# Kernel tuning notes

Measured on AMD Instinct MI355X. Metric: run time of the kernel, lower is better.

## Reference

```python
import jax, jax.numpy as jnp
import numpy as np

H = 64  # lstm hidden size
SLOPE = 0.01  # LeakyReLU default negative slope


def _leaky(x):
    return jnp.where(x >= 0, x, SLOPE * x)


def setup_inputs() -> dict:
    key = jax.random.key(0)
    ks = jax.random.split(key, 20)
    B, T = 32768, 200
    s = 0.1
    inp = {
        "noise": jax.random.normal(ks[0], (B, 3), jnp.float32),
        "w_ih0": jax.random.normal(ks[1], (4 * H, 3), jnp.float32) * s,
        "w_hh0": jax.random.normal(ks[2], (4 * H, H), jnp.float32) * s,
        "b_ih0": jax.random.normal(ks[3], (4 * H,), jnp.float32) * s,
        "b_hh0": jax.random.normal(ks[4], (4 * H,), jnp.float32) * s,
        "w_ih1": jax.random.normal(ks[5], (4 * H, H), jnp.float32) * s,
        "w_hh1": jax.random.normal(ks[6], (4 * H, H), jnp.float32) * s,
        "b_ih1": jax.random.normal(ks[7], (4 * H,), jnp.float32) * s,
        "b_hh1": jax.random.normal(ks[8], (4 * H,), jnp.float32) * s,
        "w_ih2": jax.random.normal(ks[9], (4 * H, H), jnp.float32) * s,
        "w_hh2": jax.random.normal(ks[10], (4 * H, H), jnp.float32) * s,
        "b_ih2": jax.random.normal(ks[11], (4 * H,), jnp.float32) * s,
        "b_hh2": jax.random.normal(ks[12], (4 * H,), jnp.float32) * s,
        "w1": jax.random.normal(ks[13], (32, H), jnp.float32) * s,
        "b1": jax.random.normal(ks[14], (32,), jnp.float32) * s,
        "w2": jax.random.normal(ks[15], (16, 32), jnp.float32) * s,
        "b2": jax.random.normal(ks[16], (16,), jnp.float32) * s,
        "w3": jax.random.normal(ks[17], (3, 16), jnp.float32) * s,
        "b3": jax.random.normal(ks[18], (3,), jnp.float32) * s,
        "length": T,
    }
    return inp


def _forward(noise, w_ih0, w_hh0, b_ih0, b_hh0, w_ih1, w_hh1, b_ih1, b_hh1,
             w_ih2, w_hh2, b_ih2, b_hh2, w1, b1, w2, b2, w3, b3, length):
    B = noise.shape[0]
    layers = [(w_ih0, w_hh0, b_ih0, b_hh0),
              (w_ih1, w_hh1, b_ih1, b_hh1),
              (w_ih2, w_hh2, b_ih2, b_hh2)]

    def cell(x, h, c, wih, whh, bih, bhh):
        # PyTorch LSTM gate order: i, f, g, o
        g = x @ wih.T + h @ whh.T + (bih + bhh)
        i, f, gg, o = jnp.split(g, 4, axis=-1)
        c_new = jax.nn.sigmoid(f) * c + jax.nn.sigmoid(i) * jnp.tanh(gg)
        h_new = jax.nn.sigmoid(o) * jnp.tanh(c_new)
        return h_new, c_new

    def step(carry, _):
        x, hs, cs = carry  # x: (B,3), hs/cs: (3,B,H)
        inp = x
        new_h, new_c = [], []
        for l, (wih, whh, bih, bhh) in enumerate(layers):
            h, c = cell(inp, hs[l], cs[l], wih, whh, bih, bhh)
            new_h.append(h)
            new_c.append(c)
            inp = h
        # MLP head (Dropout is identity in eval; LeakyReLU slope 0.01)
        y = _leaky(inp @ w1.T + b1)
        y = _leaky(y @ w2.T + b2)
        y = _leaky(y @ w3.T + b3)  # (B, 3)
        return (y, jnp.stack(new_h), jnp.stack(new_c)), y

    hs0 = jnp.zeros((3, B, H), noise.dtype)
    cs0 = jnp.zeros((3, B, H), noise.dtype)
    (_, _, _), ys = jax.lax.scan(step, (noise, hs0, cs0), None, length=length)
    return jnp.transpose(ys, (1, 0, 2))  # (B, T, 3)


def reference(noise, w_ih0, w_hh0, b_ih0, b_hh0, w_ih1, w_hh1, b_ih1, b_hh1,
              w_ih2, w_hh2, b_ih2, b_hh2, w1, b1, w2, b2, w3, b3, length):
    return _forward(noise, w_ih0, w_hh0, b_ih0, b_hh0, w_ih1, w_hh1, b_ih1,
                    b_hh1, w_ih2, w_hh2, b_ih2, b_hh2, w1, b1, w2, b2, w3,
                    b3, length)
```

## Files before the change

kernel.cpp:

```cpp
#include <hip/hip_runtime.h>

typedef __attribute__((ext_vector_type(4))) float  f32x4;
typedef __attribute__((ext_vector_type(8))) short  bf16x8;

#define NTHR 1024
#define BT   128
#define L2E  1.4426950408889634f

#define PLANE(L)   ((L)*16384)
#define QBUFP(p)   (49152 + ((p)<<14))
#define XFB_OFF    81920
#define Y1_OFF     83968
#define Y2_OFF     92672
#define W2L_OFF    97280
#define BGL_OFF    98304
#define B1L_OFF    101376
#define B2L_OFF    101504
#define B3L_OFF    101568
#define W3L_OFF    101584
#define W0L_OFF    101776
#define OUT_OFF    105872
#define LDS_TOTAL  112016

__device__ __align__(16) unsigned char g_wsbuf[167936];

__device__ __forceinline__ unsigned short f2bf(float v) {
    unsigned int x = __float_as_uint(v);
    unsigned int r = x + 0x7fffu + ((x >> 16) & 1u);
    return (unsigned short)(r >> 16);
}
__device__ __forceinline__ float bf2f_lo(unsigned int d) { return __uint_as_float(d << 16); }
__device__ __forceinline__ float bf2f_hi(unsigned int d) { return __uint_as_float(d & 0xffff0000u); }

__device__ __forceinline__ float fsig2(float y) {
    return __builtin_amdgcn_rcpf(1.0f + __builtin_amdgcn_exp2f(-y));
}
__device__ __forceinline__ float ftanh2(float y) {
    return 1.0f - 2.0f * __builtin_amdgcn_rcpf(1.0f + __builtin_amdgcn_exp2f(y));
}
__device__ __forceinline__ float ftanhc(float c) {
    return 1.0f - 2.0f * __builtin_amdgcn_rcpf(1.0f + __builtin_amdgcn_exp2f(c * (2.0f * L2E)));
}

__global__ void prep_weights(const float* __restrict__ whh0, const float* __restrict__ wih1,
                             const float* __restrict__ whh1, const float* __restrict__ wih2,
                             const float* __restrict__ whh2, const float* __restrict__ w1g)
{
    int gi = blockIdx.x * 256 + threadIdx.x;
    if (gi < 10240) {
        int m = gi / 2048;
        int rem = gi & 2047;
        int b = rem >> 6, l = rem & 63;
        int ks = b & 1, g = (b >> 1) & 3, ug = b >> 3;
        int row = g * 64 + ug * 16 + (l & 15);
        int kb  = ks * 32 + (l >> 4) * 8;
        float fac = (g == 2) ? (2.0f * L2E) : L2E;
        const float* src = (m == 0) ? whh0 : (m == 1) ? wih1 : (m == 2) ? whh1
                         : (m == 3) ? wih2 : whh2;
        unsigned short o[8];
        #pragma unroll
        for (int i = 0; i < 8; ++i)
            o[i] = f2bf(src[row * 64 + kb + i] * fac);
        unsigned char* dst = g_wsbuf + m * 32768 + b * 1024 + l * 16;
        #pragma unroll
        for (int i = 0; i < 8; ++i) ((unsigned short*)dst)[i] = o[i];
    } else if (gi < 10496) {
        int g2 = gi - 10240;
        int b = g2 >> 6, l = g2 & 63;
        int ks = b & 1, hf = b >> 1;
        int row = hf * 16 + (l & 15);
        int kb  = ks * 32 + (l >> 4) * 8;
        unsigned short o[8];
        #pragma unroll
        for (int i = 0; i < 8; ++i)
            o[i] = f2bf(w1g[row * 64 + kb + i]);
        unsigned char* dst = g_wsbuf + 163840 + b * 1024 + l * 16;
        #pragma unroll
        for (int i = 0; i < 8; ++i) ((unsigned short*)dst)[i] = o[i];
    }
}

#define MFMA_(A,B,C) __builtin_amdgcn_mfma_f32_16x16x32_bf16(A, B, C, 0, 0, 0)

#define BARX do { \
    asm volatile("s_waitcnt lgkmcnt(0)" ::: "memory"); \
    __builtin_amdgcn_s_barrier(); \
    __builtin_amdgcn_sched_barrier(0); \
    } while (0)

#define LOADQ(m, ks, R) \
    R = *(const bf16x8*)(g_wsbuf + (m) * 32768 + \
        ((tid >> 6) * 2 + (ks)) * 1024 + (tid & 63) * 16)
#define COMMITQ(R, p) \
    *(bf16x8*)(lds + QBUFP(p) + tid * 16) = R
#define LOADW1(R) do { if (tid < 256) \
    R = *(const bf16x8*)(g_wsbuf + 163840 + (tid >> 6) * 1024 + (tid & 63) * 16); } while (0)
#define COMMITW1(R, p) do { if (tid < 256) \
    *(bf16x8*)(lds + QBUFP(p) + tid * 16) = R; } while (0)

#define ACC_INIT(L) do { \
    _Pragma("unroll") for (int g_ = 0; g_ < 4; ++g_) { \
        float b_ = *(const float*)(lds + BGL_OFF + ((L) * 256 + g_ * 64 + u) * 4); \
        f32x4 t_ = {b_, b_, b_, b_}; \
        _Pragma("unroll") for (int mt_ = 0; mt_ < 2; ++mt_) acc[g_][mt_] = t_; \
    } } while (0)

#define GATEP(APL, ks, P) do { \
    bf16x8 b_[4]; \
    _Pragma("unroll") for (int g_ = 0; g_ < 4; ++g_) \
        b_[g_] = *(const bf16x8*)(lds + QBUFP(P) + (ug * 4 + g_) * 1024 + lane * 16); \
    _Pragma("unroll") for (int mt_ = 0; mt_ < 2; ++mt_) { \
        int ab_ = (((mbase + mt_ * 16 + l15) * 128 + (ks) * 64 + l4 * 16)) ^ rswz; \
        bf16x8 ah_ = *(const bf16x8*)(lds + PLANE(APL) + ab_); \
        _Pragma("unroll") for (int g_ = 0; g_ < 4; ++g_) \
            acc[g_][mt_] = MFMA_(ah_, b_[g_], acc[g_][mt_]); \
    } } while (0)

#define CELLW(L, CARR) do { \
    _Pragma("unroll") for (int mt_ = 0; mt_ < 2; ++mt_) \
    _Pragma("unroll") for (int r_ = 0; r_ < 4; ++r_) { \
        float gi_ = fsig2(acc[0][mt_][r_]); \
        float gf_ = fsig2(acc[1][mt_][r_]); \
        float gg_ = ftanh2(acc[2][mt_][r_]); \
        float go_ = fsig2(acc[3][mt_][r_]); \
        float cn_ = gf_ * CARR[mt_ * 4 + r_] + gi_ * gg_; \
        CARR[mt_ * 4 + r_] = cn_; \
        float hn_ = go_ * ftanhc(cn_); \
        int e_ = mbase + mt_ * 16 + l4 * 4 + r_; \
        int wb_ = ((e_ * 128 + u * 2)) ^ ((e_ & 7) << 4); \
        *(unsigned short*)(lds + PLANE(L) + wb_) = f2bf(hn_); \
    } } while (0)

#define XPART do { \
    _Pragma("unroll") for (int mt_ = 0; mt_ < 2; ++mt_) \
    _Pragma("unroll") for (int r_ = 0; r_ < 4; ++r_) { \
        int e_ = mbase + mt_ * 16 + l4 * 4 + r_; \
        f32x4 xv_ = *(const f32x4*)(lds + XFB_OFF + e_ * 16); \
        _Pragma("unroll") for (int g_ = 0; g_ < 4; ++g_) { \
            f32x4 w0_ = *(const f32x4*)(lds + W0L_OFF + (g_ * 64 + u) * 16); \
            acc[g_][mt_][r_] += xv_.x * w0_.x + xv_.y * w0_.y + xv_.z * w0_.z; \
        } } } while (0)

#define MLP1(P) do { \
    int Mt_ = wv >> 1, half_ = wv & 1; \
    float b1_ = *(const float*)(lds + B1L_OFF + (half_ * 16 + l15) * 4); \
    f32x4 a1_ = {b1_, b1_, b1_, b1_}; \
    _Pragma("unroll") for (int ks_ = 0; ks_ < 2; ++ks_) { \
        int ab_ = (((Mt_ * 16 + l15) * 128 + ks_ * 64 + l4 * 16)) ^ rswz; \
        bf16x8 ah_ = *(const bf16x8*)(lds + PLANE(2) + ab_); \
        bf16x8 wh_ = *(const bf16x8*)(lds + QBUFP(P) + (half_ * 2 + ks_) * 1024 + lane * 16); \
        a1_ = MFMA_(ah_, wh_, a1_); \
    } \
    _Pragma("unroll") for (int r_ = 0; r_ < 4; ++r_) { \
        float y_ = a1_[r_]; y_ = (y_ >= 0.f) ? y_ : 0.01f * y_; \
        int e_ = Mt_ * 16 + l4 * 4 + r_; \
        *(unsigned short*)(lds + Y1_OFF + e_ * 68 + half_ * 32 + l15 * 2) = f2bf(y_); \
    } } while (0)

#define MLP2 do { \
    int e2_ = tid & 127, rg_ = tid >> 7; \
    float a2_[2]; \
    _Pragma("unroll") for (int m_ = 0; m_ < 2; ++m_) \
        a2_[m_] = *(const float*)(lds + B2L_OFF + (rg_ * 2 + m_) * 4); \
    _Pragma("unroll") for (int kd_ = 0; kd_ < 16; ++kd_) { \
        unsigned int d_ = *(const unsigned int*)(lds + Y1_OFF + e2_ * 68 + kd_ * 4); \
        float v0_ = bf2f_lo(d_), v1_ = bf2f_hi(d_); \
        _Pragma("unroll") for (int m_ = 0; m_ < 2; ++m_) { \
            unsigned int w_ = *(const unsigned int*)(lds + W2L_OFF + ((rg_ * 2 + m_) * 32 + kd_ * 2) * 2); \
            a2_[m_] = fmaf(v0_, bf2f_lo(w_), a2_[m_]); \
            a2_[m_] = fmaf(v1_, bf2f_hi(w_), a2_[m_]); \
        } } \
    _Pragma("unroll") for (int m_ = 0; m_ < 2; ++m_) { \
        float y_ = a2_[m_]; y_ = (y_ >= 0.f) ? y_ : 0.01f * y_; \
        *(unsigned short*)(lds + Y2_OFF + e2_ * 36 + (rg_ * 2 + m_) * 2) = f2bf(y_); \
    } } while (0)

#define MLP3_OUT do { \
    if (tid < 384) { \
        int e3_ = tid & 127, r3_ = tid >> 7; \
        float a3_ = *(const float*)(lds + B3L_OFF + r3_ * 4); \
        _Pragma("unroll") for (int kd_ = 0; kd_ < 8; ++kd_) { \
            unsigned int d_ = *(const unsigned int*)(lds + Y2_OFF + e3_ * 36 + kd_ * 4); \
            a3_ = fmaf(bf2f_lo(d_), *(const float*)(lds + W3L_OFF + (r3_ * 16 + kd_ * 2) * 4),     a3_); \
            a3_ = fmaf(bf2f_hi(d_), *(const float*)(lds + W3L_OFF + (r3_ * 16 + kd_ * 2 + 1) * 4), a3_); \
        } \
        float y_ = (a3_ >= 0.f) ? a3_ : 0.01f * a3_; \
        *(float*)(lds + XFB_OFF + e3_ * 16 + r3_ * 4) = y_; \
        *(float*)(lds + OUT_OFF + e3_ * 48 + (t & 3) * 12 + r3_ * 4) = y_; \
    } } while (0)

extern "C" __global__ void __launch_bounds__(NTHR)
__attribute__((amdgpu_waves_per_eu(4, 4)))
lstm_mfma(const float* __restrict__ noise,
          const float* __restrict__ wih0, const float* __restrict__ whh0,
          const float* __restrict__ bih0, const float* __restrict__ bhh0,
          const float* __restrict__ wih1, const float* __restrict__ whh1,
          const float* __restrict__ bih1, const float* __restrict__ bhh1,
          const float* __restrict__ wih2, const float* __restrict__ whh2,
          const float* __restrict__ bih2, const float* __restrict__ bhh2,
          const float* __restrict__ w1g, const float* __restrict__ b1g,
          const float* __restrict__ w2g, const float* __restrict__ b2g,
          const float* __restrict__ w3g, const float* __restrict__ b3g,
          const int* __restrict__ lenp, float* __restrict__ out)
{
    extern __shared__ unsigned char lds[];
    const int tid  = threadIdx.x;
    const int lane = tid & 63;
    const int wv   = tid >> 6;
    const int ug   = wv & 3;
    const int mh   = wv >> 2;
    const int l15  = lane & 15;
    const int l4   = lane >> 4;
    const int u    = ug * 16 + l15;
    const int mbase = mh * 32;
    const int rswz  = (lane & 7) << 4;
    const int T = *lenp;
    const long eg0  = (long)blockIdx.x * BT;
    const long outs = 3L * T;

    float c0[8], c1[8], c2[8];
    #pragma unroll
    for (int i = 0; i < 8; ++i) { c0[i] = 0.f; c1[i] = 0.f; c2[i] = 0.f; }

    bf16x8 RA, RB, RC;

    LOADQ(0, 0, RA);
    LOADQ(0, 1, RB);
    LOADQ(1, 0, RC);

    for (int i = tid; i < 49152 / 4; i += NTHR) ((unsigned int*)lds)[i] = 0u;
    if (tid < BT) {
        const float* np = noise + (eg0 + tid) * 3;
        f32x4 xv = {np[0], np[1], np[2], 0.f};
        *(f32x4*)(lds + XFB_OFF + tid * 16) = xv;
    }
    if (tid < 512) *(unsigned short*)(lds + W2L_OFF + tid * 2) = f2bf(w2g[tid]);
    if (tid < 768) {
        int l = tid >> 8, r = tid & 255, g = r >> 6;
        float fac = (g == 2) ? (2.0f * L2E) : L2E;
        const float* bi = (l == 0) ? bih0 : ((l == 1) ? bih1 : bih2);
        const float* bh = (l == 0) ? bhh0 : ((l == 1) ? bhh1 : bhh2);
        *(float*)(lds + BGL_OFF + tid * 4) = (bi[r] + bh[r]) * fac;
    }
    if (tid < 256) {
        int g = tid >> 6;
        float fac = (g == 2) ? (2.0f * L2E) : L2E;
        f32x4 wv0 = {wih0[tid * 3] * fac, wih0[tid * 3 + 1] * fac,
                     wih0[tid * 3 + 2] * fac, 0.f};
        *(f32x4*)(lds + W0L_OFF + tid * 16) = wv0;
    }
    if (tid < 32) *(float*)(lds + B1L_OFF + tid * 4) = b1g[tid];
    if (tid < 16) *(float*)(lds + B2L_OFF + tid * 4) = b2g[tid];
    if (tid < 3)  *(float*)(lds + B3L_OFF + tid * 4) = b3g[tid];
    if (tid < 48) *(float*)(lds + W3L_OFF + tid * 4) = w3g[tid];

    __syncthreads();
    COMMITQ(RA, 0);
    __syncthreads();

    f32x4 acc[4][2];

    #pragma unroll 1
    for (int t = 0; t < T; ++t) {
        const int bp = t & 1;
        COMMITQ(RB, bp ^ 1); LOADQ(1, 1, RA);
        ACC_INIT(0); XPART;
        GATEP(0, 0, bp);
        BARX;
        COMMITQ(RC, bp); LOADQ(2, 0, RB);
        GATEP(0, 1, bp ^ 1);
        BARX;
        CELLW(0, c0);
        BARX;
        COMMITQ(RA, bp ^ 1); LOADQ(2, 1, RC);
        ACC_INIT(1);
        GATEP(0, 0, bp);
        BARX;
        COMMITQ(RB, bp); LOADQ(3, 0, RA);
        GATEP(0, 1, bp ^ 1);
        BARX;
        COMMITQ(RC, bp ^ 1); LOADQ(3, 1, RB);
        GATEP(1, 0, bp);
        BARX;
        COMMITQ(RA, bp); LOADQ(4, 0, RC);
        GATEP(1, 1, bp ^ 1);
        BARX;
        CELLW(1, c1);
        BARX;
        COMMITQ(RB, bp ^ 1); LOADQ(4, 1, RA);
        ACC_INIT(2);
        GATEP(1, 0, bp);
        BARX;
        COMMITQ(RC, bp); LOADW1(RB);
        GATEP(1, 1, bp ^ 1);
        BARX;
        COMMITQ(RA, bp ^ 1); LOADQ(0, 0, RC);
        GATEP(2, 0, bp);
        BARX;
        COMMITW1(RB, bp); LOADQ(0, 1, RA);
        GATEP(2, 1, bp ^ 1);
        BARX;
        CELLW(2, c2);
        BARX;
        COMMITQ(RC, bp ^ 1); LOADQ(1, 0, RB);
        MLP1(bp);
        BARX;
        MLP2;
        BARX;
        MLP3_OUT;
        if ((t & 3) == 3) {
            BARX;
            long tb = t - 3;
            #pragma unroll
            for (int it = 0; it < 2; ++it) {
                int i = it * NTHR + tid;
                if (i < 1536) {
                    int e = i / 12, j = i - e * 12;
                    out[(eg0 + e) * outs + tb * 3 + j] =
                        *(const float*)(lds + OUT_OFF + e * 48 + j * 4);
                }
            }
        }
        BARX;
        { bf16x8 tmp = RB; RB = RA; RC = tmp; }
    }

    int nst = T & 3;
    if (nst) {
        int nfl = BT * nst * 3;
        for (int i = tid; i < nfl; i += NTHR) {
            int e = i / (nst * 3), j = i - e * (nst * 3);
            out[(eg0 + e) * outs + (long)(T - nst) * 3 + j] =
                *(const float*)(lds + OUT_OFF + e * 48 + j * 4);
        }
    }
}

extern "C" void kernel_launch(void* const* d_in, const int* in_sizes, int n_in,
                              void* d_out, int out_size, void* d_ws, size_t ws_size,
                              hipStream_t stream)
{
    const float* noise = (const float*)d_in[0];
    const float* wih0  = (const float*)d_in[1];
    const float* whh0  = (const float*)d_in[2];
    const float* bih0  = (const float*)d_in[3];
    const float* bhh0  = (const float*)d_in[4];
    const float* wih1  = (const float*)d_in[5];
    const float* whh1  = (const float*)d_in[6];
    const float* bih1  = (const float*)d_in[7];
    const float* bhh1  = (const float*)d_in[8];
    const float* wih2  = (const float*)d_in[9];
    const float* whh2  = (const float*)d_in[10];
    const float* bih2  = (const float*)d_in[11];
    const float* bhh2  = (const float*)d_in[12];
    const float* w1g   = (const float*)d_in[13];
    const float* b1g   = (const float*)d_in[14];
    const float* w2g   = (const float*)d_in[15];
    const float* b2g   = (const float*)d_in[16];
    const float* w3g   = (const float*)d_in[17];
    const float* b3g   = (const float*)d_in[18];
    const int*   lenp  = (const int*)d_in[19];
    float* out = (float*)d_out;

    int B = in_sizes[0] / 3;
    int grid = B / BT;

    prep_weights<<<41, 256, 0, stream>>>(whh0, wih1, whh1, wih2, whh2, w1g);

    hipFuncSetAttribute((const void*)lstm_mfma,
                        hipFuncAttributeMaxDynamicSharedMemorySize, LDS_TOTAL);
    lstm_mfma<<<grid, NTHR, LDS_TOTAL, stream>>>(
        noise, wih0, whh0, bih0, bhh0, wih1, whh1, bih1, bhh1,
        wih2, whh2, bih2, bhh2, w1g, b1g, w2g, b2g, w3g, b3g, lenp, out);
}
```

Measured before the change: 3.957 ms.

## Stream whole weight matrices per stage to halve LDS barriers in LSTM step

Weight staging changes from half-matrix (one k-slice) chunks to full 64x256 matrices double-buffered in LDS (two 32KB buffers). Each gate product now performs both k-slices in one GATEM call, which roughly halves the number of block-wide barriers per timestep and removes the register rotation. The cost is more LDS (about 145KB total), two live bf16x8 register pairs per thread, and larger global loads issued per stage, which may reduce latency hiding.

```diff
diff --git a/kernel.cpp b/kernel.cpp
--- a/kernel.cpp
+++ b/kernel.cpp
@@ -8,19 +8,20 @@
 #define L2E  1.4426950408889634f
 
 #define PLANE(L)   ((L)*16384)
-#define QBUFP(p)   (49152 + ((p)<<14))
-#define XFB_OFF    81920
-#define Y1_OFF     83968
-#define Y2_OFF     92672
-#define W2L_OFF    97280
-#define BGL_OFF    98304
-#define B1L_OFF    101376
-#define B2L_OFF    101504
-#define B3L_OFF    101568
-#define W3L_OFF    101584
-#define W0L_OFF    101776
-#define OUT_OFF    105872
-#define LDS_TOTAL  112016
+#define QB0        49152
+#define QB1        81920
+#define XFB_OFF    114688
+#define Y1_OFF     116736
+#define Y2_OFF     125440
+#define W2L_OFF    130048
+#define BGL_OFF    131072
+#define B1L_OFF    134144
+#define B2L_OFF    134272
+#define B3L_OFF    134336
+#define W3L_OFF    134352
+#define W0L_OFF    134544
+#define OUT_OFF    138640
+#define LDS_TOTAL  144784
 
 __device__ __align__(16) unsigned char g_wsbuf[167936];
 
@@ -88,15 +89,18 @@
     __builtin_amdgcn_sched_barrier(0); \
     } while (0)
 
-#define LOADQ(m, ks, R) \
-    R = *(const bf16x8*)(g_wsbuf + (m) * 32768 + \
-        ((tid >> 6) * 2 + (ks)) * 1024 + (tid & 63) * 16)
-#define COMMITQ(R, p) \
-    *(bf16x8*)(lds + QBUFP(p) + tid * 16) = R
-#define LOADW1(R) do { if (tid < 256) \
-    R = *(const bf16x8*)(g_wsbuf + 163840 + (tid >> 6) * 1024 + (tid & 63) * 16); } while (0)
-#define COMMITW1(R, p) do { if (tid < 256) \
-    *(bf16x8*)(lds + QBUFP(p) + tid * 16) = R; } while (0)
+#define LOADM(m, R0, R1) do { \
+    R0 = *(const bf16x8*)(g_wsbuf + (m) * 32768 + ((tid >> 6) * 2 + 0) * 1024 + (tid & 63) * 16); \
+    R1 = *(const bf16x8*)(g_wsbuf + (m) * 32768 + ((tid >> 6) * 2 + 1) * 1024 + (tid & 63) * 16); \
+    } while (0)
+#define COMMITM(R0, R1, B) do { \
+    *(bf16x8*)(lds + (B) + ((tid >> 6) * 2 + 0) * 1024 + (tid & 63) * 16) = R0; \
+    *(bf16x8*)(lds + (B) + ((tid >> 6) * 2 + 1) * 1024 + (tid & 63) * 16) = R1; \
+    } while (0)
+#define LOADW1(R0) do { if (tid < 256) \
+    R0 = *(const bf16x8*)(g_wsbuf + 163840 + (tid >> 6) * 1024 + (tid & 63) * 16); } while (0)
+#define COMMITW1(R0, B) do { if (tid < 256) \
+    *(bf16x8*)(lds + (B) + (tid >> 6) * 1024 + (tid & 63) * 16) = R0; } while (0)
 
 #define ACC_INIT(L) do { \
     _Pragma("unroll") for (int g_ = 0; g_ < 4; ++g_) { \
@@ -105,16 +109,19 @@
         _Pragma("unroll") for (int mt_ = 0; mt_ < 2; ++mt_) acc[g_][mt_] = t_; \
     } } while (0)
 
-#define GATEP(APL, ks, P) do { \
-    bf16x8 b_[4]; \
+#define GATEM(APL, B) do { \
+    bf16x8 b_[8]; \
     _Pragma("unroll") for (int g_ = 0; g_ < 4; ++g_) \
-        b_[g_] = *(const bf16x8*)(lds + QBUFP(P) + (ug * 4 + g_) * 1024 + lane * 16); \
+    _Pragma("unroll") for (int ks_ = 0; ks_ < 2; ++ks_) \
+        b_[g_ * 2 + ks_] = *(const bf16x8*)(lds + (B) + ((ug * 4 + g_) * 2 + ks_) * 1024 + lane * 16); \
     _Pragma("unroll") for (int mt_ = 0; mt_ < 2; ++mt_) { \
-        int ab_ = (((mbase + mt_ * 16 + l15) * 128 + (ks) * 64 + l4 * 16)) ^ rswz; \
-        bf16x8 ah_ = *(const bf16x8*)(lds + PLANE(APL) + ab_); \
-        _Pragma("unroll") for (int g_ = 0; g_ < 4; ++g_) \
-            acc[g_][mt_] = MFMA_(ah_, b_[g_], acc[g_][mt_]); \
-    } } while (0)
+        int ar_ = (mbase + mt_ * 16 + l15) * 128 + l4 * 16; \
+        bf16x8 ah0_ = *(const bf16x8*)(lds + PLANE(APL) + ((ar_      ) ^ rswz)); \
+        bf16x8 ah1_ = *(const bf16x8*)(lds + PLANE(APL) + ((ar_ +  64) ^ rswz)); \
+        _Pragma("unroll") for (int g_ = 0; g_ < 4; ++g_) { \
+            acc[g_][mt_] = MFMA_(ah0_, b_[g_ * 2 + 0], acc[g_][mt_]); \
+            acc[g_][mt_] = MFMA_(ah1_, b_[g_ * 2 + 1], acc[g_][mt_]); \
+        } } } while (0)
 
 #define CELLW(L, CARR) do { \
     _Pragma("unroll") for (int mt_ = 0; mt_ < 2; ++mt_) \
@@ -141,14 +148,14 @@
             acc[g_][mt_][r_] += xv_.x * w0_.x + xv_.y * w0_.y + xv_.z * w0_.z; \
         } } } while (0)
 
-#define MLP1(P) do { \
+#define MLP1(B) do { \
     int Mt_ = wv >> 1, half_ = wv & 1; \
     float b1_ = *(const float*)(lds + B1L_OFF + (half_ * 16 + l15) * 4); \
     f32x4 a1_ = {b1_, b1_, b1_, b1_}; \
     _Pragma("unroll") for (int ks_ = 0; ks_ < 2; ++ks_) { \
         int ab_ = (((Mt_ * 16 + l15) * 128 + ks_ * 64 + l4 * 16)) ^ rswz; \
         bf16x8 ah_ = *(const bf16x8*)(lds + PLANE(2) + ab_); \
-        bf16x8 wh_ = *(const bf16x8*)(lds + QBUFP(P) + (half_ * 2 + ks_) * 1024 + lane * 16); \
+        bf16x8 wh_ = *(const bf16x8*)(lds + (B) + (half_ * 2 + ks_) * 1024 + lane * 16); \
         a1_ = MFMA_(ah_, wh_, a1_); \
     } \
     _Pragma("unroll") for (int r_ = 0; r_ < 4; ++r_) { \
@@ -222,11 +229,10 @@
     #pragma unroll
     for (int i = 0; i < 8; ++i) { c0[i] = 0.f; c1[i] = 0.f; c2[i] = 0.f; }
 
-    bf16x8 RA, RB, RC;
-
-    LOADQ(0, 0, RA);
-    LOADQ(0, 1, RB);
-    LOADQ(1, 0, RC);
+    bf16x8 RA0, RA1, RB0, RB1;
+
+    LOADM(0, RA0, RA1);
+    LOADM(1, RB0, RB1);
 
     for (int i = tid; i < 49152 / 4; i += NTHR) ((unsigned int*)lds)[i] = 0u;
     if (tid < BT) {
@@ -255,55 +261,39 @@
     if (tid < 48) *(float*)(lds + W3L_OFF + tid * 4) = w3g[tid];
 
     __syncthreads();
-    COMMITQ(RA, 0);
+    COMMITM(RA0, RA1, QB0);
     __syncthreads();
 
     f32x4 acc[4][2];
 
     #pragma unroll 1
     for (int t = 0; t < T; ++t) {
-        const int bp = t & 1;
-        COMMITQ(RB, bp ^ 1); LOADQ(1, 1, RA);
+        COMMITM(RB0, RB1, QB1); LOADM(2, RA0, RA1);
         ACC_INIT(0); XPART;
-        GATEP(0, 0, bp);
-        BARX;
-        COMMITQ(RC, bp); LOADQ(2, 0, RB);
-        GATEP(0, 1, bp ^ 1);
-        BARX;
+        GATEM(0, QB0);
+        BARX;
+        COMMITM(RA0, RA1, QB0); LOADM(3, RB0, RB1);
         CELLW(0, c0);
         BARX;
-        COMMITQ(RA, bp ^ 1); LOADQ(2, 1, RC);
         ACC_INIT(1);
-        GATEP(0, 0, bp);
-        BARX;
-        COMMITQ(RB, bp); LOADQ(3, 0, RA);
-        GATEP(0, 1, bp ^ 1);
-        BARX;
-        COMMITQ(RC, bp ^ 1); LOADQ(3, 1, RB);
-        GATEP(1, 0, bp);
-        BARX;
-        COMMITQ(RA, bp); LOADQ(4, 0, RC);
-        GATEP(1, 1, bp ^ 1);
-        BARX;
+        GATEM(0, QB1);
+        BARX;
+        COMMITM(RB0, RB1, QB1); LOADM(4, RA0, RA1);
+        GATEM(1, QB0);
+        BARX;
+        COMMITM(RA0, RA1, QB0); LOADW1(RB0);
         CELLW(1, c1);
         BARX;
-        COMMITQ(RB, bp ^ 1); LOADQ(4, 1, RA);
         ACC_INIT(2);
-        GATEP(1, 0, bp);
-        BARX;
-        COMMITQ(RC, bp); LOADW1(RB);
-        GATEP(1, 1, bp ^ 1);
-        BARX;
-        COMMITQ(RA, bp ^ 1); LOADQ(0, 0, RC);
-        GATEP(2, 0, bp);
-        BARX;
-        COMMITW1(RB, bp); LOADQ(0, 1, RA);
-        GATEP(2, 1, bp ^ 1);
-        BARX;
+        GATEM(1, QB1);
+        BARX;
+        COMMITW1(RB0, QB1); LOADM(0, RA0, RA1);
+        GATEM(2, QB0);
+        BARX;
+        COMMITM(RA0, RA1, QB0); LOADM(1, RB0, RB1);
         CELLW(2, c2);
         BARX;
-        COMMITQ(RC, bp ^ 1); LOADQ(1, 0, RB);
-        MLP1(bp);
+        MLP1(QB1);
         BARX;
         MLP2;
         BARX;
@@ -322,7 +312,6 @@
             }
         }
         BARX;
-        { bf16x8 tmp = RB; RB = RA; RC = tmp; }
     }
 
     int nst = T & 3;
```

After: 4.237 ms. 1.07x slower.

## Overlap next-step layer-0 recurrent GEMM with MLP head and use MFMA for MLP2

Applied to the files above, without the earlier changes.

Layer-0's hidden-state GEMM for the next timestep is moved into the tail of the current step, where it interleaves with the MLP head, and the separate LOADW1/COMMITW1 barrier stage is removed. The MLP weights w1 and w2 are now held in registers as bf16 MFMA fragments, and layer 2 of the MLP runs as one MFMA per wave instead of scalar FMAs. The aim is to cut the number of barriers per step and shorten the serial per-step critical path. It costs extra register pressure, and the rotated weight-staging buffer schedule has to stay exactly consistent.

```diff
diff --git a/kernel.cpp b/kernel.cpp
--- a/kernel.cpp
+++ b/kernel.cpp
@@ -2,27 +2,26 @@
 
 typedef __attribute__((ext_vector_type(4))) float  f32x4;
 typedef __attribute__((ext_vector_type(8))) short  bf16x8;
+typedef __attribute__((ext_vector_type(4))) short  bf16x4;
 
 #define NTHR 1024
 #define BT   128
 #define L2E  1.4426950408889634f
 
 #define PLANE(L)   ((L)*16384)
-#define QBUFP(p)   (49152 + ((p)<<14))
+#define QB0        49152
+#define QB1        65536
 #define XFB_OFF    81920
 #define Y1_OFF     83968
-#define Y2_OFF     92672
-#define W2L_OFF    97280
-#define BGL_OFF    98304
-#define B1L_OFF    101376
-#define B2L_OFF    101504
-#define B3L_OFF    101568
-#define W3L_OFF    101584
-#define W0L_OFF    101776
-#define OUT_OFF    105872
-#define LDS_TOTAL  112016
-
-__device__ __align__(16) unsigned char g_wsbuf[167936];
+#define Y2_OFF     93184
+#define BGL_OFF    97792
+#define W0L_OFF    100864
+#define B3L_OFF    104960
+#define W3L_OFF    104976
+#define OUT_OFF    105168
+#define LDS_TOTAL  111312
+
+__device__ __align__(16) unsigned char g_wsbuf[163840];
 
 __device__ __forceinline__ unsigned short f2bf(float v) {
     unsigned int x = __float_as_uint(v);
@@ -44,7 +43,7 @@
 
 __global__ void prep_weights(const float* __restrict__ whh0, const float* __restrict__ wih1,
                              const float* __restrict__ whh1, const float* __restrict__ wih2,
-                             const float* __restrict__ whh2, const float* __restrict__ w1g)
+                             const float* __restrict__ whh2)
 {
     int gi = blockIdx.x * 256 + threadIdx.x;
     if (gi < 10240) {
@@ -64,19 +63,6 @@
         unsigned char* dst = g_wsbuf + m * 32768 + b * 1024 + l * 16;
         #pragma unroll
         for (int i = 0; i < 8; ++i) ((unsigned short*)dst)[i] = o[i];
-    } else if (gi < 10496) {
-        int g2 = gi - 10240;
-        int b = g2 >> 6, l = g2 & 63;
-        int ks = b & 1, hf = b >> 1;
-        int row = hf * 16 + (l & 15);
-        int kb  = ks * 32 + (l >> 4) * 8;
-        unsigned short o[8];
-        #pragma unroll
-        for (int i = 0; i < 8; ++i)
-            o[i] = f2bf(w1g[row * 64 + kb + i]);
-        unsigned char* dst = g_wsbuf + 163840 + b * 1024 + l * 16;
-        #pragma unroll
-        for (int i = 0; i < 8; ++i) ((unsigned short*)dst)[i] = o[i];
     }
 }
 
@@ -91,24 +77,20 @@
 #define LOADQ(m, ks, R) \
     R = *(const bf16x8*)(g_wsbuf + (m) * 32768 + \
         ((tid >> 6) * 2 + (ks)) * 1024 + (tid & 63) * 16)
-#define COMMITQ(R, p) \
-    *(bf16x8*)(lds + QBUFP(p) + tid * 16) = R
-#define LOADW1(R) do { if (tid < 256) \
-    R = *(const bf16x8*)(g_wsbuf + 163840 + (tid >> 6) * 1024 + (tid & 63) * 16); } while (0)
-#define COMMITW1(R, p) do { if (tid < 256) \
-    *(bf16x8*)(lds + QBUFP(p) + tid * 16) = R; } while (0)
+#define COMMITQ(R, BUF) \
+    *(bf16x8*)(lds + (BUF) + tid * 16) = R
 
 #define ACC_INIT(L) do { \
     _Pragma("unroll") for (int g_ = 0; g_ < 4; ++g_) { \
         float b_ = *(const float*)(lds + BGL_OFF + ((L) * 256 + g_ * 64 + u) * 4); \
         f32x4 t_ = {b_, b_, b_, b_}; \
-        _Pragma("unroll") for (int mt_ = 0; mt_ < 2; ++mt_) acc[g_][mt_] = t_; \
-    } } while (0)
-
-#define GATEP(APL, ks, P) do { \
+        acc[g_][0] = t_; acc[g_][1] = t_; \
+    } } while (0)
+
+#define GATEP(APL, ks, BUF) do { \
     bf16x8 b_[4]; \
     _Pragma("unroll") for (int g_ = 0; g_ < 4; ++g_) \
-        b_[g_] = *(const bf16x8*)(lds + QBUFP(P) + (ug * 4 + g_) * 1024 + lane * 16); \
+        b_[g_] = *(const bf16x8*)(lds + (BUF) + (ug * 4 + g_) * 1024 + lane * 16); \
     _Pragma("unroll") for (int mt_ = 0; mt_ < 2; ++mt_) { \
         int ab_ = (((mbase + mt_ * 16 + l15) * 128 + (ks) * 64 + l4 * 16)) ^ rswz; \
         bf16x8 ah_ = *(const bf16x8*)(lds + PLANE(APL) + ab_); \
@@ -141,39 +123,34 @@
             acc[g_][mt_][r_] += xv_.x * w0_.x + xv_.y * w0_.y + xv_.z * w0_.z; \
         } } } while (0)
 
-#define MLP1(P) do { \
-    int Mt_ = wv >> 1, half_ = wv & 1; \
-    float b1_ = *(const float*)(lds + B1L_OFF + (half_ * 16 + l15) * 4); \
-    f32x4 a1_ = {b1_, b1_, b1_, b1_}; \
-    _Pragma("unroll") for (int ks_ = 0; ks_ < 2; ++ks_) { \
-        int ab_ = (((Mt_ * 16 + l15) * 128 + ks_ * 64 + l4 * 16)) ^ rswz; \
-        bf16x8 ah_ = *(const bf16x8*)(lds + PLANE(2) + ab_); \
-        bf16x8 wh_ = *(const bf16x8*)(lds + QBUFP(P) + (half_ * 2 + ks_) * 1024 + lane * 16); \
-        a1_ = MFMA_(ah_, wh_, a1_); \
-    } \
+#define MLP1 do { \
+    int Mt_ = wv >> 1; \
+    f32x4 a1_ = {b1r, b1r, b1r, b1r}; \
+    { int ab_ = (((Mt_ * 16 + l15) * 128 + 0 * 64 + l4 * 16)) ^ rswz; \
+      bf16x8 ah_ = *(const bf16x8*)(lds + PLANE(2) + ab_); \
+      a1_ = MFMA_(ah_, w1f0, a1_); } \
+    { int ab_ = (((Mt_ * 16 + l15) * 128 + 1 * 64 + l4 * 16)) ^ rswz; \
+      bf16x8 ah_ = *(const bf16x8*)(lds + PLANE(2) + ab_); \
+      a1_ = MFMA_(ah_, w1f1, a1_); } \
     _Pragma("unroll") for (int r_ = 0; r_ < 4; ++r_) { \
         float y_ = a1_[r_]; y_ = (y_ >= 0.f) ? y_ : 0.01f * y_; \
         int e_ = Mt_ * 16 + l4 * 4 + r_; \
-        *(unsigned short*)(lds + Y1_OFF + e_ * 68 + half_ * 32 + l15 * 2) = f2bf(y_); \
-    } } while (0)
-
-#define MLP2 do { \
-    int e2_ = tid & 127, rg_ = tid >> 7; \
-    float a2_[2]; \
-    _Pragma("unroll") for (int m_ = 0; m_ < 2; ++m_) \
-        a2_[m_] = *(const float*)(lds + B2L_OFF + (rg_ * 2 + m_) * 4); \
-    _Pragma("unroll") for (int kd_ = 0; kd_ < 16; ++kd_) { \
-        unsigned int d_ = *(const unsigned int*)(lds + Y1_OFF + e2_ * 68 + kd_ * 4); \
-        float v0_ = bf2f_lo(d_), v1_ = bf2f_hi(d_); \
-        _Pragma("unroll") for (int m_ = 0; m_ < 2; ++m_) { \
-            unsigned int w_ = *(const unsigned int*)(lds + W2L_OFF + ((rg_ * 2 + m_) * 32 + kd_ * 2) * 2); \
-            a2_[m_] = fmaf(v0_, bf2f_lo(w_), a2_[m_]); \
-            a2_[m_] = fmaf(v1_, bf2f_hi(w_), a2_[m_]); \
-        } } \
-    _Pragma("unroll") for (int m_ = 0; m_ < 2; ++m_) { \
-        float y_ = a2_[m_]; y_ = (y_ >= 0.f) ? y_ : 0.01f * y_; \
-        *(unsigned short*)(lds + Y2_OFF + e2_ * 36 + (rg_ * 2 + m_) * 2) = f2bf(y_); \
-    } } while (0)
+        *(unsigned short*)(lds + Y1_OFF + e_ * 72 + hf * 32 + l15 * 2) = f2bf(y_); \
+    } } while (0)
+
+#define MLP2M do { \
+    if (wv < 8) { \
+        bf16x4 alo_ = *(const bf16x4*)(lds + Y1_OFF + (wv * 16 + l15) * 72 + l4 * 16); \
+        bf16x4 ahi_ = *(const bf16x4*)(lds + Y1_OFF + (wv * 16 + l15) * 72 + l4 * 16 + 8); \
+        bf16x8 af_ = {alo_[0], alo_[1], alo_[2], alo_[3], \
+                      ahi_[0], ahi_[1], ahi_[2], ahi_[3]}; \
+        f32x4 a2_ = {b2r, b2r, b2r, b2r}; \
+        a2_ = MFMA_(af_, w2f, a2_); \
+        _Pragma("unroll") for (int r_ = 0; r_ < 4; ++r_) { \
+            float y_ = a2_[r_]; y_ = (y_ >= 0.f) ? y_ : 0.01f * y_; \
+            int e_ = wv * 16 + l4 * 4 + r_; \
+            *(unsigned short*)(lds + Y2_OFF + e_ * 36 + l15 * 2) = f2bf(y_); \
+        } } } while (0)
 
 #define MLP3_OUT do { \
     if (tid < 384) { \
@@ -214,6 +191,7 @@
     const int u    = ug * 16 + l15;
     const int mbase = mh * 32;
     const int rswz  = (lane & 7) << 4;
+    const int hf    = wv & 1;
     const int T = *lenp;
     const long eg0  = (long)blockIdx.x * BT;
     const long outs = 3L * T;
@@ -222,11 +200,28 @@
     #pragma unroll
     for (int i = 0; i < 8; ++i) { c0[i] = 0.f; c1[i] = 0.f; c2[i] = 0.f; }
 
-    bf16x8 RA, RB, RC;
-
-    LOADQ(0, 0, RA);
-    LOADQ(0, 1, RB);
-    LOADQ(1, 0, RC);
+    bf16x8 w1f0, w1f1, w2f;
+    {
+        const float* p0 = w1g + (hf * 16 + l15) * 64 + l4 * 8;
+        w1f0 = (bf16x8){(short)f2bf(p0[0]), (short)f2bf(p0[1]), (short)f2bf(p0[2]),
+                        (short)f2bf(p0[3]), (short)f2bf(p0[4]), (short)f2bf(p0[5]),
+                        (short)f2bf(p0[6]), (short)f2bf(p0[7])};
+        const float* p1 = p0 + 32;
+        w1f1 = (bf16x8){(short)f2bf(p1[0]), (short)f2bf(p1[1]), (short)f2bf(p1[2]),
+                        (short)f2bf(p1[3]), (short)f2bf(p1[4]), (short)f2bf(p1[5]),
+                        (short)f2bf(p1[6]), (short)f2bf(p1[7])};
+        const float* p2 = w2g + l15 * 32 + l4 * 8;
+        w2f  = (bf16x8){(short)f2bf(p2[0]), (short)f2bf(p2[1]), (short)f2bf(p2[2]),
+                        (short)f2bf(p2[3]), (short)f2bf(p2[4]), (short)f2bf(p2[5]),
+                        (short)f2bf(p2[6]), (short)f2bf(p2[7])};
+    }
+    const float b1r = b1g[hf * 16 + l15];
+    const float b2r = b2g[l15];
+
+    bf16x8 RB, RC, RT;
+    LOADQ(1, 0, RT);
+    LOADQ(1, 1, RB);
+    LOADQ(2, 0, RC);
 
     for (int i = tid; i < 49152 / 4; i += NTHR) ((unsigned int*)lds)[i] = 0u;
     if (tid < BT) {
@@ -234,7 +229,6 @@
         f32x4 xv = {np[0], np[1], np[2], 0.f};
         *(f32x4*)(lds + XFB_OFF + tid * 16) = xv;
     }
-    if (tid < 512) *(unsigned short*)(lds + W2L_OFF + tid * 2) = f2bf(w2g[tid]);
     if (tid < 768) {
         int l = tid >> 8, r = tid & 255, g = r >> 6;
         float fac = (g == 2) ? (2.0f * L2E) : L2E;
@@ -249,63 +243,59 @@
                      wih0[tid * 3 + 2] * fac, 0.f};
         *(f32x4*)(lds + W0L_OFF + tid * 16) = wv0;
     }
-    if (tid < 32) *(float*)(lds + B1L_OFF + tid * 4) = b1g[tid];
-    if (tid < 16) *(float*)(lds + B2L_OFF + tid * 4) = b2g[tid];
     if (tid < 3)  *(float*)(lds + B3L_OFF + tid * 4) = b3g[tid];
     if (tid < 48) *(float*)(lds + W3L_OFF + tid * 4) = w3g[tid];
 
     __syncthreads();
-    COMMITQ(RA, 0);
+    COMMITQ(RT, QB0);
+
+    f32x4 acc[4][2];
+    ACC_INIT(0);
     __syncthreads();
-
-    f32x4 acc[4][2];
 
     #pragma unroll 1
     for (int t = 0; t < T; ++t) {
-        const int bp = t & 1;
-        COMMITQ(RB, bp ^ 1); LOADQ(1, 1, RA);
-        ACC_INIT(0); XPART;
-        GATEP(0, 0, bp);
-        BARX;
-        COMMITQ(RC, bp); LOADQ(2, 0, RB);
-        GATEP(0, 1, bp ^ 1);
-        BARX;
+        XPART;
         CELLW(0, c0);
         BARX;
-        COMMITQ(RA, bp ^ 1); LOADQ(2, 1, RC);
+        COMMITQ(RB, QB1); LOADQ(2, 1, RB);
         ACC_INIT(1);
-        GATEP(0, 0, bp);
-        BARX;
-        COMMITQ(RB, bp); LOADQ(3, 0, RA);
-        GATEP(0, 1, bp ^ 1);
-        BARX;
-        COMMITQ(RC, bp ^ 1); LOADQ(3, 1, RB);
-        GATEP(1, 0, bp);
-        BARX;
-        COMMITQ(RA, bp); LOADQ(4, 0, RC);
-        GATEP(1, 1, bp ^ 1);
+        GATEP(0, 0, QB0);
+        BARX;
+        COMMITQ(RC, QB0); LOADQ(3, 0, RC);
+        GATEP(0, 1, QB1);
+        BARX;
+        COMMITQ(RB, QB1); LOADQ(3, 1, RB);
+        GATEP(1, 0, QB0);
+        BARX;
+        COMMITQ(RC, QB0); LOADQ(4, 0, RC);
+        GATEP(1, 1, QB1);
         BARX;
         CELLW(1, c1);
         BARX;
-        COMMITQ(RB, bp ^ 1); LOADQ(4, 1, RA);
+        COMMITQ(RB, QB1); LOADQ(4, 1, RB);
         ACC_INIT(2);
-        GATEP(1, 0, bp);
-        BARX;
-        COMMITQ(RC, bp); LOADW1(RB);
-        GATEP(1, 1, bp ^ 1);
-        BARX;
-        COMMITQ(RA, bp ^ 1); LOADQ(0, 0, RC);
-        GATEP(2, 0, bp);
-        BARX;
-        COMMITW1(RB, bp); LOADQ(0, 1, RA);
-        GATEP(2, 1, bp ^ 1);
+        GATEP(1, 0, QB0);
+        BARX;
+        COMMITQ(RC, QB0); LOADQ(0, 0, RC);
+        GATEP(1, 1, QB1);
+        BARX;
+        COMMITQ(RB, QB1); LOADQ(0, 1, RB);
+        GATEP(2, 0, QB0);
+        BARX;
+        COMMITQ(RC, QB0); LOADQ(1, 0, RC);
+        GATEP(2, 1, QB1);
         BARX;
         CELLW(2, c2);
         BARX;
-        COMMITQ(RC, bp ^ 1); LOADQ(1, 0, RB);
-        MLP1(bp);
-        BARX;
-        MLP2;
+        COMMITQ(RB, QB1); LOADQ(1, 1, RB);
+        MLP1;
+        ACC_INIT(0);
+        GATEP(0, 0, QB0);
+        BARX;
+        COMMITQ(RC, QB0); LOADQ(2, 0, RC);
+        MLP2M;
+        GATEP(0, 1, QB1);
         BARX;
         MLP3_OUT;
         if ((t & 3) == 3) {
@@ -322,7 +312,6 @@
             }
         }
         BARX;
-        { bf16x8 tmp = RB; RB = RA; RC = tmp; }
     }
 
     int nst = T & 3;
@@ -365,7 +354,7 @@
     int B = in_sizes[0] / 3;
     int grid = B / BT;
 
-    prep_weights<<<41, 256, 0, stream>>>(whh0, wih1, whh1, wih2, whh2, w1g);
+    prep_weights<<<40, 256, 0, stream>>>(whh0, wih1, whh1, wih2, whh2);
 
     hipFuncSetAttribute((const void*)lstm_mfma,
                         hipFuncAttributeMaxDynamicSharedMemorySize, LDS_TOTAL);
```

After: 3.681 ms. 1.07x faster.
